# Optimization experiments

Hardware: AMD Instinct MI355X
Metric: run time of the kernel (lower is better)

## Reference

```python
import jax, jax.numpy as jnp
import numpy as np

N, F, HID, H, B = 400000, 128, 32, 4, 2000

def setup_inputs() -> dict:
    key = jax.random.key(0)
    ks = jax.random.split(key, 8)
    atom_fea = jax.random.normal(ks[0], (N, F), dtype=jnp.float32)
    segment_ids = jnp.sort(jax.random.randint(ks[1], (N,), 0, B, dtype=jnp.int32))
    s = 0.05
    return {
        "atom_fea": atom_fea,
        "segment_ids": segment_ids,
        "num_crystals": B,
        "W1": jax.random.normal(ks[2], (F, HID), dtype=jnp.float32) * s,
        "b1": jnp.zeros((HID,), dtype=jnp.float32),
        "W2": jax.random.normal(ks[3], (HID, H), dtype=jnp.float32) * s,
        "b2": jnp.zeros((H,), dtype=jnp.float32),
        "Wp": jax.random.normal(ks[4], (H * F, F), dtype=jnp.float32) * s,
        "bp": jnp.zeros((F,), dtype=jnp.float32),
    }

def reference(atom_fea, segment_ids, num_crystals, W1, b1, W2, b2, Wp, bp):
    # key MLP: (N,F) -> (N,H) attention logits (dropout is eval no-op)
    logits = jax.nn.silu(atom_fea @ W1 + b1) @ W2 + b2  # (N,H)
    # segment softmax over atoms within each crystal, per head
    seg_max = jax.ops.segment_max(logits, segment_ids, num_segments=num_crystals)
    ex = jnp.exp(logits - seg_max[segment_ids])
    denom = jax.ops.segment_sum(ex, segment_ids, num_segments=num_crystals)
    w = ex / denom[segment_ids]  # (N,H)
    # per-head softmax-weighted segment sum of atom features -> (B,H,F)
    weighted = jax.ops.segment_sum(
        w[:, :, None] * atom_fea[:, None, :], segment_ids, num_segments=num_crystals
    )
    flat = weighted.reshape(num_crystals, -1)  # (B, H*F)
    return jax.nn.silu(flat @ Wp + bp)  # (B,F)
```

## Files before the change

### kernel.cpp

```cpp
#include <hip/hip_runtime.h>
#include <math.h>

#define F 128
#define HID 32
#define NH 4
#define TILE 32
#define ROWB 512

typedef __attribute__((ext_vector_type(8))) short bf16x8;
typedef __attribute__((ext_vector_type(4))) float f32x4;

__device__ __forceinline__ float silu_f(float x) {
    return x / (1.0f + __expf(-x));
}

__device__ __forceinline__ uint f2bf(float f) {
    union { float f; uint u; } v; v.f = f;
    uint r = v.u + 0x7fffu + ((v.u >> 16) & 1u);
    return r >> 16;
}

__device__ __forceinline__ uint cvtpk_bf16(float lo, float hi) {
    uint r;
    asm("v_cvt_pk_bf16_f32 %0, %1, %2" : "=v"(r) : "v"(lo), "v"(hi));
    return r;
}

__device__ __forceinline__ void gload_lds16(const void* g, void* l) {
    __builtin_amdgcn_global_load_lds(
        (const __attribute__((address_space(1))) void*)g,
        (__attribute__((address_space(3))) void*)l, 16, 0, 0);
}

__device__ __forceinline__ int lower_bound_wave(const int* __restrict__ seg, int N,
                                                int v, int lane) {
    int lo = 0, hi = N;
    while (hi - lo > 64) {
        const int step = ((hi - lo) + 63) >> 6;
        const int idx = lo + lane * step;
        const bool inr = (idx < hi);
        const int val = inr ? seg[idx] : 0;
        const unsigned long long m = __ballot(inr && (val < v));
        const int cnt = __popcll(m);
        if (cnt == 0) return lo;
        const int probe_hi = lo + cnt * step;
        lo = lo + (cnt - 1) * step + 1;
        hi = (probe_hi < hi) ? probe_hi : hi;
    }
    const int idx = lo + lane;
    const bool inr = (idx < hi);
    const int val = inr ? seg[idx] : 0;
    const unsigned long long m = __ballot(inr && (val < v));
    return lo + __popcll(m);
}

__global__ __launch_bounds__(256, 4) void fused17_kernel(
    const float* __restrict__ atom_fea, const int* __restrict__ seg, int N,
    const float* __restrict__ W1, const float* __restrict__ b1,
    const float* __restrict__ W2, const float* __restrict__ b2,
    const float* __restrict__ Wp, const float* __restrict__ bp,
    float* __restrict__ out) {
    __shared__ float sStage[2][TILE * F];
    __shared__ float sP[2 * TILE * 5];
    __shared__ float sTW[NH * 65];

    const int t = threadIdx.x;
    const int b = blockIdx.x;
    const int wv = t >> 6;
    const int lane = t & 63;
    const int lg = lane >> 4;
    const int l15 = lane & 15;
    const int ag = wv & 1;
    const int mh = wv >> 1;
    const int ca = lane & 3;
    const int co = (lane >> 2) & 15;

    const int start = lower_bound_wave(seg, N, b, lane);
    const int end = lower_bound_wave(seg, N, b + 1, lane);

    int roff[4], coff[4];
    #pragma unroll
    for (int i = 0; i < 4; ++i) {
        const int q = i * 256 + t;
        roff[i] = q >> 5;
        coff[i] = ((q & 31) ^ (roff[i] & 7)) << 4;
    }

    bf16x8 w1f[4];
    #pragma unroll
    for (int kk = 0; kk < 4; ++kk) {
        bf16x8 fr;
        #pragma unroll
        for (int j = 0; j < 8; ++j)
            fr[j] = (short)f2bf(W1[(kk * 32 + lg * 8 + j) * HID + mh * 16 + l15]);
        w1f[kk] = fr;
    }
    float b1r[4], w2r[4][4];
    #pragma unroll
    for (int r = 0; r < 4; ++r) {
        const int h = mh * 16 + lg * 4 + r;
        b1r[r] = b1[h];
        #pragma unroll
        for (int j = 0; j < 4; ++j) w2r[r][j] = W2[h * NH + j];
    }
    const float b2w = b2[wv];

    float m_run = -INFINITY;
    float s_part = 0.0f;
    float acc8[8] = {0, 0, 0, 0, 0, 0, 0, 0};

    const int nt = (end > start) ? (end - start + TILE - 1) / TILE : 0;
    const char* gbase = (const char*)atom_fea;

    if (nt > 0) {
        #pragma unroll
        for (int i = 0; i < 4; ++i) {
            int a = start + roff[i]; a = (a < end) ? a : end - 1;
            gload_lds16(gbase + (size_t)a * ROWB + coff[i],
                        (char*)sStage[0] + i * 4096 + wv * 1024);
        }
    }
    __syncthreads();

    int pb = 0;
    for (int ti = 0; ti < nt; ++ti) {
        const int base = start + ti * TILE;
        const int T = min(TILE, end - base);
        const char* bufc = (const char*)sStage[pb];
        const bool has_next = (ti + 1 < nt);

        if (has_next) {
            const int nbase = base + TILE;
            char* ldst = (char*)sStage[pb ^ 1];
            #pragma unroll
            for (int i = 0; i < 4; ++i) {
                int a = nbase + roff[i]; a = (a < end) ? a : end - 1;
                gload_lds16(gbase + (size_t)a * ROWB + coff[i],
                            ldst + i * 4096 + wv * 1024);
            }
        }

        {
            f32x4 acc;
            #pragma unroll
            for (int r = 0; r < 4; ++r) acc[r] = b1r[r];
            const int row = ag * 16 + l15;
            const char* rb = bufc + row * ROWB;
            const int rs = row & 7;
            #pragma unroll
            for (int kk = 0; kk < 4; ++kk) {
                const int c0 = kk * 8 + lg * 2;
                const float4 va = *(const float4*)(rb + ((c0 ^ rs) << 4));
                const float4 vb = *(const float4*)(rb + (((c0 + 1) ^ rs) << 4));
                union { bf16x8 v; uint u[4]; } fr;
                fr.u[0] = cvtpk_bf16(va.x, va.y);
                fr.u[1] = cvtpk_bf16(va.z, va.w);
                fr.u[2] = cvtpk_bf16(vb.x, vb.y);
                fr.u[3] = cvtpk_bf16(vb.z, vb.w);
                acc = __builtin_amdgcn_mfma_f32_16x16x32_bf16(w1f[kk], fr.v, acc, 0, 0, 0);
            }
            float p0 = 0, p1 = 0, p2 = 0, p3 = 0;
            #pragma unroll
            for (int r = 0; r < 4; ++r) {
                const float s = silu_f(acc[r]);
                p0 = fmaf(s, w2r[r][0], p0);
                p1 = fmaf(s, w2r[r][1], p1);
                p2 = fmaf(s, w2r[r][2], p2);
                p3 = fmaf(s, w2r[r][3], p3);
            }
            p0 += __shfl_xor(p0, 16); p0 += __shfl_xor(p0, 32);
            p1 += __shfl_xor(p1, 16); p1 += __shfl_xor(p1, 32);
            p2 += __shfl_xor(p2, 16); p2 += __shfl_xor(p2, 32);
            p3 += __shfl_xor(p3, 16); p3 += __shfl_xor(p3, 32);
            if (lane < 16) {
                float* d = &sP[(mh * TILE + ag * 16 + lane) * 5];
                d[0] = p0; d[1] = p1; d[2] = p2; d[3] = p3;
            }
        }
        asm volatile("s_waitcnt lgkmcnt(0)" ::: "memory");
        __builtin_amdgcn_s_barrier();

        {
            const float v = (lane < T)
                ? sP[lane * 5 + wv] + sP[(TILE + lane) * 5 + wv] + b2w
                : -INFINITY;
            if (__any(v > m_run + 8.0f)) {
                float mt = v;
                #pragma unroll
                for (int d = 1; d < 64; d <<= 1) mt = fmaxf(mt, __shfl_xor(mt, d));
                const float m_new = fmaxf(m_run, mt);
                const float r = __expf(m_run - m_new);
                s_part *= r;
                #pragma unroll
                for (int j = 0; j < 8; ++j) acc8[j] *= r;
                m_run = m_new;
            }
            const float e = (lane < T) ? __expf(v - m_run) : 0.0f;
            sTW[wv * 65 + lane] = e;
            s_part += e;
        }

        {
            #pragma unroll 4
            for (int i = 0; i < 8; ++i) {
                const int a = i * 4 + ca;
                const float w = sTW[wv * 65 + a];
                const int sw = a & 7;
                const char* ra = bufc + a * ROWB;
                const float4 v0 = *(const float4*)(ra + (((2 * co) ^ sw) << 4));
                const float4 v1 = *(const float4*)(ra + (((2 * co + 1) ^ sw) << 4));
                acc8[0] = fmaf(w, v0.x, acc8[0]);
                acc8[1] = fmaf(w, v0.y, acc8[1]);
                acc8[2] = fmaf(w, v0.z, acc8[2]);
                acc8[3] = fmaf(w, v0.w, acc8[3]);
                acc8[4] = fmaf(w, v1.x, acc8[4]);
                acc8[5] = fmaf(w, v1.y, acc8[5]);
                acc8[6] = fmaf(w, v1.z, acc8[6]);
                acc8[7] = fmaf(w, v1.w, acc8[7]);
            }
        }
        __syncthreads();
        pb ^= 1;
    }

    #pragma unroll
    for (int d = 1; d < 64; d <<= 1) s_part += __shfl_xor(s_part, d);
    const float inv = (s_part > 0.0f) ? 1.0f / s_part : 0.0f;
    #pragma unroll
    for (int j = 0; j < 8; ++j) {
        acc8[j] += __shfl_xor(acc8[j], 1);
        acc8[j] += __shfl_xor(acc8[j], 2);
    }
    float* sWacc = (float*)sStage;
    float* sPart = (float*)sStage + 512;
    if ((lane & 3) == 0) {
        float* dst = &sWacc[wv * F + (lane >> 2) * 8];
        dst[0] = acc8[0] * inv; dst[1] = acc8[1] * inv;
        dst[2] = acc8[2] * inv; dst[3] = acc8[3] * inv;
        dst[4] = acc8[4] * inv; dst[5] = acc8[5] * inv;
        dst[6] = acc8[6] * inv; dst[7] = acc8[7] * inv;
    }
    __syncthreads();

    {
        const int f = t & 127, half = t >> 7;
        float sum = 0.0f;
        const float* wp = Wp + (size_t)(half * 256) * F + f;
        const float* wa = &sWacc[half * 256];
        for (int k0 = 0; k0 < 256; k0 += 8) {
            float wpv[8];
            #pragma unroll
            for (int u = 0; u < 8; ++u) wpv[u] = wp[(size_t)(k0 + u) * F];
            #pragma unroll
            for (int u = 0; u < 8; ++u) sum = fmaf(wa[k0 + u], wpv[u], sum);
        }
        sPart[t] = sum;
    }
    __syncthreads();
    if (t < 128) out[(size_t)b * F + t] = silu_f(sPart[t] + sPart[t + 128] + bp[t]);
}

extern "C" void kernel_launch(void* const* d_in, const int* in_sizes, int n_in,
                              void* d_out, int out_size, void* d_ws, size_t ws_size,
                              hipStream_t stream) {
    const float* atom_fea = (const float*)d_in[0];
    const int* seg = (const int*)d_in[1];
    const float* W1 = (const float*)d_in[3];
    const float* b1 = (const float*)d_in[4];
    const float* W2 = (const float*)d_in[5];
    const float* b2 = (const float*)d_in[6];
    const float* Wp = (const float*)d_in[7];
    const float* bp = (const float*)d_in[8];
    float* out = (float*)d_out;

    const int N = in_sizes[0] / F;
    const int B = out_size / F;

    fused17_kernel<<<B, 256, 0, stream>>>(atom_fea, seg, N, W1, b1, W2, b2, Wp, bp, out);
}
```

Baseline: 61.66 us.

## Split weighted-sum work by atom across waves instead of by head

Previously each wave handled one head and read all 32 atoms of a tile from LDS for the weighted feature sum. Now each wave handles 8 atoms across all 4 heads, with lanes mapped to head × feature-chunk. Each wave keeps its own per-head running max and sum, and a new epilogue merges the four waves' partial softmax states through an extra LDS buffer. This cuts the LDS row reads per wave and the full-wave max reductions, at the cost of a cross-wave merge step and more shared memory, which may lower occupancy.

New measurement: 68.83 us. 11.6% more time.

```diff
diff --git a/kernel.cpp b/kernel.cpp
--- a/kernel.cpp
+++ b/kernel.cpp
@@ -54,7 +54,7 @@
     return lo + __popcll(m);
 }
 
-__global__ __launch_bounds__(256, 4) void fused17_kernel(
+__global__ __launch_bounds__(256, 4) void fused19_kernel(
     const float* __restrict__ atom_fea, const int* __restrict__ seg, int N,
     const float* __restrict__ W1, const float* __restrict__ b1,
     const float* __restrict__ W2, const float* __restrict__ b2,
@@ -62,7 +62,8 @@
     float* __restrict__ out) {
     __shared__ float sStage[2][TILE * F];
     __shared__ float sP[2 * TILE * 5];
-    __shared__ float sTW[NH * 65];
+    __shared__ float sTW[NH][8 * NH];
+    __shared__ float sEpi[NH][520];
 
     const int t = threadIdx.x;
     const int b = blockIdx.x;
@@ -72,8 +73,9 @@
     const int l15 = lane & 15;
     const int ag = wv & 1;
     const int mh = wv >> 1;
-    const int ca = lane & 3;
-    const int co = (lane >> 2) & 15;
+    const int ch = lane & 3;
+    const int ao = (lane >> 2) & 7;
+    const int co = lane >> 2;
 
     const int start = lower_bound_wave(seg, N, b, lane);
     const int end = lower_bound_wave(seg, N, b + 1, lane);
@@ -103,10 +105,11 @@
         #pragma unroll
         for (int j = 0; j < 4; ++j) w2r[r][j] = W2[h * NH + j];
     }
-    const float b2w = b2[wv];
+    const float b2r0 = b2[0], b2r1 = b2[1], b2r2 = b2[2], b2r3 = b2[3];
+    const float b2h = (ch & 1) ? ((ch & 2) ? b2r3 : b2r1) : ((ch & 2) ? b2r2 : b2r0);
 
     float m_run = -INFINITY;
-    float s_part = 0.0f;
+    float s_run = 0.0f;
     float acc8[8] = {0, 0, 0, 0, 0, 0, 0, 0};
 
     const int nt = (end > start) ? (end - start + TILE - 1) / TILE : 0;
@@ -181,30 +184,34 @@
         __builtin_amdgcn_s_barrier();
 
         {
-            const float v = (lane < T)
-                ? sP[lane * 5 + wv] + sP[(TILE + lane) * 5 + wv] + b2w
+            const int a = wv * 8 + ao;
+            const bool valid = (a < T);
+            const float v = valid
+                ? sP[a * 5 + ch] + sP[(TILE + a) * 5 + ch] + b2h
                 : -INFINITY;
             if (__any(v > m_run + 8.0f)) {
                 float mt = v;
-                #pragma unroll
-                for (int d = 1; d < 64; d <<= 1) mt = fmaxf(mt, __shfl_xor(mt, d));
+                mt = fmaxf(mt, __shfl_xor(mt, 4));
+                mt = fmaxf(mt, __shfl_xor(mt, 8));
+                mt = fmaxf(mt, __shfl_xor(mt, 16));
+                mt = fmaxf(mt, __shfl_xor(mt, 32));
                 const float m_new = fmaxf(m_run, mt);
                 const float r = __expf(m_run - m_new);
-                s_part *= r;
+                s_run *= r;
                 #pragma unroll
                 for (int j = 0; j < 8; ++j) acc8[j] *= r;
                 m_run = m_new;
             }
-            const float e = (lane < T) ? __expf(v - m_run) : 0.0f;
-            sTW[wv * 65 + lane] = e;
-            s_part += e;
+            const float e = valid ? __expf(v - m_run) : 0.0f;
+            if (lane < 32) sTW[wv][ao * NH + ch] = e;
+            s_run += e;
         }
 
         {
             #pragma unroll 4
             for (int i = 0; i < 8; ++i) {
-                const int a = i * 4 + ca;
-                const float w = sTW[wv * 65 + a];
+                const int a = wv * 8 + i;
+                const float w = sTW[wv][i * NH + ch];
                 const int sw = a & 7;
                 const char* ra = bufc + a * ROWB;
                 const float4 v0 = *(const float4*)(ra + (((2 * co) ^ sw) << 4));
@@ -223,22 +230,45 @@
         pb ^= 1;
     }
 
-    #pragma unroll
-    for (int d = 1; d < 64; d <<= 1) s_part += __shfl_xor(s_part, d);
-    const float inv = (s_part > 0.0f) ? 1.0f / s_part : 0.0f;
-    #pragma unroll
-    for (int j = 0; j < 8; ++j) {
-        acc8[j] += __shfl_xor(acc8[j], 1);
-        acc8[j] += __shfl_xor(acc8[j], 2);
-    }
+    s_run += __shfl_xor(s_run, 4);
+    s_run += __shfl_xor(s_run, 8);
+    s_run += __shfl_xor(s_run, 16);
+
+    *(float4*)&sEpi[wv][lane * 8] = make_float4(acc8[0], acc8[1], acc8[2], acc8[3]);
+    *(float4*)&sEpi[wv][lane * 8 + 4] = make_float4(acc8[4], acc8[5], acc8[6], acc8[7]);
+    if (lane < 4) {
+        sEpi[wv][512 + lane] = m_run;
+        sEpi[wv][516 + lane] = s_run;
+    }
+    __syncthreads();
     float* sWacc = (float*)sStage;
     float* sPart = (float*)sStage + 512;
-    if ((lane & 3) == 0) {
-        float* dst = &sWacc[wv * F + (lane >> 2) * 8];
-        dst[0] = acc8[0] * inv; dst[1] = acc8[1] * inv;
-        dst[2] = acc8[2] * inv; dst[3] = acc8[3] * inv;
-        dst[4] = acc8[4] * inv; dst[5] = acc8[5] * inv;
-        dst[6] = acc8[6] * inv; dst[7] = acc8[7] * inv;
+    if (t < 64) {
+        const int ch2 = t & 3, co2 = t >> 2;
+        float mw[NH], fw[NH];
+        float mg = -INFINITY;
+        #pragma unroll
+        for (int w = 0; w < NH; ++w) {
+            mw[w] = sEpi[w][512 + ch2];
+            mg = fmaxf(mg, mw[w]);
+        }
+        float sg = 0.0f;
+        #pragma unroll
+        for (int w = 0; w < NH; ++w) {
+            fw[w] = (mw[w] == -INFINITY) ? 0.0f : __expf(mw[w] - mg);
+            sg += sEpi[w][516 + ch2] * fw[w];
+        }
+        const float inv = (sg > 0.0f) ? 1.0f / sg : 0.0f;
+        float o[8] = {0, 0, 0, 0, 0, 0, 0, 0};
+        #pragma unroll
+        for (int w = 0; w < NH; ++w) {
+            const float* ap = &sEpi[w][t * 8];
+            #pragma unroll
+            for (int j = 0; j < 8; ++j) o[j] = fmaf(ap[j], fw[w], o[j]);
+        }
+        float* dst = &sWacc[ch2 * F + co2 * 8];
+        #pragma unroll
+        for (int j = 0; j < 8; ++j) dst[j] = o[j] * inv;
     }
     __syncthreads();
 
@@ -276,5 +306,5 @@
     const int N = in_sizes[0] / F;
     const int B = out_size / F;
 
-    fused17_kernel<<<B, 256, 0, stream>>>(atom_fea, seg, N, W1, b1, W2, b2, Wp, bp, out);
-}
+    fused19_kernel<<<B, 256, 0, stream>>>(atom_fea, seg, N, W1, b1, W2, b2, Wp, bp, out);
+}
```
